# Kernel optimization log

Measured on AMD Instinct MI355X. Metric: run time of the kernel, lower is better.

## Reference

```python
import jax, jax.numpy as jnp
import numpy as np

B = 128          # graphs per batch
NP = 1024        # nodes per graph
FIN = 128        # input node features
H = 128          # hidden width (SAGEConv out)
C = 10           # output classes
N = B * NP
DEG = 16
E = N * DEG
K1 = int(np.ceil(0.8 * NP))   # 820
K2 = int(np.ceil(0.8 * K1))   # 656
K3 = int(np.ceil(0.8 * K2))   # 525


def setup_inputs() -> dict:
    key = jax.random.key(0)
    k = jax.random.split(key, 16)
    x = jax.random.normal(k[0], (N, FIN), jnp.float32)
    # edges constrained within each graph (PyG batched-graph semantics)
    g = jnp.arange(E, dtype=jnp.int32) // (E // B)
    src = g * NP + jax.random.randint(k[1], (E,), 0, NP, jnp.int32)
    dst = g * NP + jax.random.randint(k[2], (E,), 0, NP, jnp.int32)
    edge_index = jnp.stack([src, dst])

    def lin(kk, o, i):
        return jax.random.normal(kk, (o, i), jnp.float32) / np.sqrt(i)

    return {
        'x': x, 'edge_index': edge_index,
        'Wl1': lin(k[3], H, FIN), 'bl1': jnp.zeros((H,), jnp.float32), 'Wr1': lin(k[4], H, FIN),
        'wp1': jax.random.normal(k[5], (H,), jnp.float32),
        'Wl2': lin(k[6], H, H), 'bl2': jnp.zeros((H,), jnp.float32), 'Wr2': lin(k[7], H, H),
        'wp2': jax.random.normal(k[8], (H,), jnp.float32),
        'Wl3': lin(k[9], H, H), 'bl3': jnp.zeros((H,), jnp.float32), 'Wr3': lin(k[10], H, H),
        'wp3': jax.random.normal(k[11], (H,), jnp.float32),
        'Wf1': lin(k[12], 64, H), 'bf1': jnp.zeros((64,), jnp.float32),
        'Wf2': lin(k[13], C, 64), 'bf2': jnp.zeros((C,), jnp.float32),
    }


def _sage(x, src, dst, em, Wl, bl, Wr):
    # PyG SAGEConv: lin_l(mean_{j in N(i)} x_j) + lin_r(x_i); edge mask em kills pruned edges
    msg = x[src] * em[:, None]                                   # [E,H] gather
    s = jax.ops.segment_sum(msg, dst, num_segments=N)            # scatter-add
    deg = jax.ops.segment_sum(em, dst, num_segments=N)
    mean = s / jnp.maximum(deg, 1.0)[:, None]
    return mean @ Wl.T + bl + x @ Wr.T


def _topk(x, w, nm, kk):
    # TopKPooling: score = x.w/||w||, keep top ceil(ratio*n) per graph, gate kept nodes by tanh(score)
    score = (x @ w) / (jnp.linalg.norm(w) + 1e-16)               # [N]
    s2 = jnp.where(nm, score, -jnp.inf).reshape(B, NP)
    _, idx = jax.lax.top_k(s2, kk)                               # [B,kk] static shape
    sel = jnp.zeros((B, NP), bool).at[jnp.arange(B)[:, None], idx].set(True).reshape(-1)
    x = jnp.where(sel[:, None], x * jnp.tanh(score)[:, None], 0.0)
    return x, sel


def _forward(x, Wl1, bl1, Wr1, wp1, Wl2, bl2, Wr2, wp2, Wl3, bl3, Wr3, wp3,
             Wf1, bf1, Wf2, bf2, edge_index):
    src, dst = edge_index[0], edge_index[1]
    nm = jnp.ones((N,), bool)                 # node alive mask
    em = jnp.ones((E,), jnp.float32)          # edge alive mask
    for (Wl, bl, Wr, wp, kk) in ((Wl1, bl1, Wr1, wp1, K1),
                                 (Wl2, bl2, Wr2, wp2, K2),
                                 (Wl3, bl3, Wr3, wp3, K3)):
        x = jax.nn.relu(_sage(x, src, dst, em, Wl, bl, Wr))
        x, nm = _topk(x, wp, nm, kk)
        em = (nm[src] & nm[dst]).astype(jnp.float32)
    # global_mean_pool over surviving nodes per graph (pruned nodes are exactly zero)
    cnt = nm.reshape(B, NP).sum(1).astype(x.dtype)
    pooled = x.reshape(B, NP, H).sum(1) / jnp.maximum(cnt, 1.0)[:, None]
    h = jax.nn.relu(pooled @ Wf1.T + bf1)
    return jax.nn.log_softmax(h @ Wf2.T + bf2, axis=-1)


def reference(x, edge_index, Wl1, bl1, Wr1, wp1, Wl2, bl2, Wr2, wp2,
              Wl3, bl3, Wr3, wp3, Wf1, bf1, Wf2, bf2):
    return _forward(x, Wl1, bl1, Wr1, wp1, Wl2, bl2, Wr2, wp2,
                    Wl3, bl3, Wr3, wp3, Wf1, bf1, Wf2, bf2, edge_index)
```

## Files before the change

### kernel.cpp

```cpp
#include <hip/hip_runtime.h>

constexpr int NGPH = 128;
constexpr int NPG  = 1024;
constexpr int NN   = NGPH * NPG;
constexpr int HD   = 128;
constexpr int EPG  = 16384;
constexpr int KS1 = 820, KS2 = 656, KS3 = 525;

typedef _Float16 half8v __attribute__((ext_vector_type(8)));
typedef float f32x4 __attribute__((ext_vector_type(4)));

__global__ __launch_bounds__(256) void init_gate(float* __restrict__ gate) {
  int i = blockIdx.x * 256 + threadIdx.x;
  if (i < NN) gate[i] = 1.0f;
}

__global__ __launch_bounds__(256) void wconv(const float* __restrict__ Wl0, const float* __restrict__ Wr0,
                                             const float* __restrict__ Wl1, const float* __restrict__ Wr1,
                                             const float* __restrict__ Wl2, const float* __restrict__ Wr2,
                                             _Float16* __restrict__ Wc) {
  int tid = blockIdx.x * 256 + threadIdx.x;
  int layer = tid >> 15;
  int idx = tid & 32767;
  int n = idx >> 8, k = idx & 255;
  const float* Wlp = layer == 0 ? Wl0 : layer == 1 ? Wl1 : Wl2;
  const float* Wrp = layer == 0 ? Wr0 : layer == 1 ? Wr1 : Wr2;
  float v = (k < 128) ? Wlp[n * 128 + k] : Wrp[n * 128 + k - 128];
  _Float16 h = (_Float16)v;
  _Float16 l = (_Float16)(v - (float)h);
  size_t base = (size_t)layer * 65536;
  Wc[base + (size_t)n * 256 + k] = h;
  Wc[base + 32768 + (size_t)n * 256 + k] = l;
}

__global__ __launch_bounds__(512) void csr_build(int* __restrict__ ei) {
  __shared__ unsigned int ed[EPG];
  __shared__ int cnt[NPG];
  __shared__ int scn[NPG];
  __shared__ int off[NPG];
  int g = blockIdx.x, t = threadIdx.x;
  const int* srcg = ei + (size_t)g * EPG;
  const int* dstg = ei + (size_t)NGPH * EPG + (size_t)g * EPG;
  for (int i = t; i < EPG; i += 512) {
    unsigned int s = (unsigned int)(srcg[i] - (g << 10));
    unsigned int d = (unsigned int)(dstg[i] - (g << 10));
    ed[i] = s | (d << 10);
  }
  for (int i = t; i < NPG; i += 512) cnt[i] = 0;
  __syncthreads();
  for (int i = t; i < EPG; i += 512) atomicAdd(&cnt[ed[i] >> 10], 1);
  __syncthreads();
  int* a = cnt; int* b = scn;
  for (int d = 1; d < NPG; d <<= 1) {
    for (int i = t; i < NPG; i += 512) b[i] = a[i] + (i >= d ? a[i - d] : 0);
    __syncthreads();
    int* tmp = a; a = b; b = tmp;
  }
  unsigned short* ssort = (unsigned short*)(ei + (size_t)g * EPG);
  unsigned short* rsout = ssort + EPG;
  for (int r = t; r < NPG; r += 512) {
    int ex = r ? a[r - 1] : 0;
    rsout[r] = (unsigned short)ex;
    off[r] = ex;
  }
  __syncthreads();
  for (int i = t; i < EPG; i += 512) {
    unsigned int e = ed[i];
    int pos = atomicAdd(&off[e >> 10], 1);
    ssort[pos] = (unsigned short)(e & 1023u);
  }
}

__global__ __launch_bounds__(256) void agg2_kernel(const float* __restrict__ X,
                                                   const int* __restrict__ ei,
                                                   const float* __restrict__ gate,
                                                   float* __restrict__ Mout) {
  int t = threadIdx.x;
  int xcd = blockIdx.x & 7, q = blockIdx.x >> 3;
  int g = ((q >> 7) << 3) + xcd;
  int r = (q & 127) * 8 + (t >> 5);
  int lane = t & 31;
  const unsigned short* ss  = (const unsigned short*)(ei + (size_t)g * EPG);
  const unsigned short* rsg = ss + EPG;
  int start = rsg[r];
  int end   = (r < 1023) ? (int)rsg[r + 1] : EPG;
  const float4* X4 = (const float4*)X;
  size_t gb4 = (size_t)(g << 10) * 32;
  float4 acc = make_float4(0.f, 0.f, 0.f, 0.f);
  float degf = 0.f;
  for (int base = start; base < end; base += 32) {
    int ec = end - base; if (ec > 32) ec = 32;
    int sl = 0; float gv = 0.f;
    if (lane < ec) {
      sl = ss[base + lane];
      gv = gate[(g << 10) + sl];
    }
    degf += (gv != 0.f) ? 1.f : 0.f;
    int e = 0;
    for (; e + 8 <= ec; e += 8) {
      int s[8]; float gg[8]; float4 v[8];
#pragma unroll
      for (int k = 0; k < 8; ++k) { s[k] = __shfl(sl, e + k, 32); gg[k] = __shfl(gv, e + k, 32); }
#pragma unroll
      for (int k = 0; k < 8; ++k) v[k] = X4[gb4 + (size_t)s[k] * 32 + lane];
#pragma unroll
      for (int k = 0; k < 8; ++k) {
        acc.x += v[k].x * gg[k]; acc.y += v[k].y * gg[k];
        acc.z += v[k].z * gg[k]; acc.w += v[k].w * gg[k];
      }
    }
    for (; e + 4 <= ec; e += 4) {
      int s[4]; float gg[4]; float4 v[4];
#pragma unroll
      for (int k = 0; k < 4; ++k) { s[k] = __shfl(sl, e + k, 32); gg[k] = __shfl(gv, e + k, 32); }
#pragma unroll
      for (int k = 0; k < 4; ++k) v[k] = X4[gb4 + (size_t)s[k] * 32 + lane];
#pragma unroll
      for (int k = 0; k < 4; ++k) {
        acc.x += v[k].x * gg[k]; acc.y += v[k].y * gg[k];
        acc.z += v[k].z * gg[k]; acc.w += v[k].w * gg[k];
      }
    }
    for (; e < ec; ++e) {
      int s0 = __shfl(sl, e, 32);
      float g0 = __shfl(gv, e, 32);
      float4 v0 = X4[gb4 + (size_t)s0 * 32 + lane];
      acc.x += v0.x * g0; acc.y += v0.y * g0;
      acc.z += v0.z * g0; acc.w += v0.w * g0;
    }
  }
#pragma unroll
  for (int m = 1; m <= 16; m <<= 1) degf += __shfl_xor(degf, m, 32);
  float inv = 1.0f / fmaxf(degf, 1.0f);
  acc.x *= inv; acc.y *= inv; acc.z *= inv; acc.w *= inv;
  ((float4*)Mout)[(size_t)((g << 10) + r) * 32 + lane] = acc;
}

constexpr int LDA = 34;
__global__ __launch_bounds__(256, 4) void gemm_mfma(const float* S,
                                                    const float* __restrict__ X,
                                                    const _Float16* __restrict__ Wc,
                                                    const float* __restrict__ bb,
                                                    const float* __restrict__ wp,
                                                    const float* __restrict__ gate,
                                                    float* Hout,
                                                    float* __restrict__ score) {
  __shared__ _Float16 Ah[128 * LDA];
  __shared__ _Float16 Al[128 * LDA];
  __shared__ _Float16 Bh[128 * LDA];
  __shared__ _Float16 Bl[128 * LDA];
  __shared__ float sc_s[128];
  int t = threadIdx.x;
  int r0 = blockIdx.x * 128;
  int lane = t & 63, wid = t >> 6;
  int wm = wid & 1, wn = wid >> 1;
  int quad = lane >> 4, mr = lane & 15;
  const _Float16* WH = Wc;
  const _Float16* WL = Wc + 32768;

  f32x4 acc[4][4];
#pragma unroll
  for (int i = 0; i < 4; ++i)
#pragma unroll
    for (int j = 0; j < 4; ++j) acc[i][j] = (f32x4){0.f, 0.f, 0.f, 0.f};

  for (int ks = 0; ks < 256; ks += 32) {
    bool isS = (ks < 128);
    const float* Asrc = isS ? (S + (size_t)r0 * HD + ks)
                            : (X + (size_t)r0 * HD + (ks - 128));
#pragma unroll
    for (int i = 0; i < 2; ++i) {
      int slot = t + i * 256;
      int row = slot >> 2;
      int kq = (slot & 3) * 8;
      float4 v0 = *(const float4*)&Asrc[(size_t)row * HD + kq];
      float4 v1 = *(const float4*)&Asrc[(size_t)row * HD + kq + 4];
      if (!isS) {
        float gv = gate[r0 + row];
        v0.x *= gv; v0.y *= gv; v0.z *= gv; v0.w *= gv;
        v1.x *= gv; v1.y *= gv; v1.z *= gv; v1.w *= gv;
      }
      half8v h, l;
      h[0] = (_Float16)v0.x; h[1] = (_Float16)v0.y; h[2] = (_Float16)v0.z; h[3] = (_Float16)v0.w;
      h[4] = (_Float16)v1.x; h[5] = (_Float16)v1.y; h[6] = (_Float16)v1.z; h[7] = (_Float16)v1.w;
      l[0] = (_Float16)(v0.x - (float)h[0]); l[1] = (_Float16)(v0.y - (float)h[1]);
      l[2] = (_Float16)(v0.z - (float)h[2]); l[3] = (_Float16)(v0.w - (float)h[3]);
      l[4] = (_Float16)(v1.x - (float)h[4]); l[5] = (_Float16)(v1.y - (float)h[5]);
      l[6] = (_Float16)(v1.z - (float)h[6]); l[7] = (_Float16)(v1.w - (float)h[7]);
      *(half8v*)&Ah[row * LDA + kq] = h;
      *(half8v*)&Al[row * LDA + kq] = l;
    }
#pragma unroll
    for (int i = 0; i < 2; ++i) {
      int slot = t + i * 256;
      int n = slot >> 2;
      int kq = (slot & 3) * 8;
      *(half8v*)&Bh[n * LDA + kq] = *(const half8v*)&WH[(size_t)n * 256 + ks + kq];
      *(half8v*)&Bl[n * LDA + kq] = *(const half8v*)&WL[(size_t)n * 256 + ks + kq];
    }
    __syncthreads();
    half8v af[4], alf[4], bf[4], blf[4];
#pragma unroll
    for (int i = 0; i < 4; ++i) {
      int rowA = (wm * 64 + i * 16 + mr) * LDA + quad * 8;
      af[i]  = *(const half8v*)&Ah[rowA];
      alf[i] = *(const half8v*)&Al[rowA];
    }
#pragma unroll
    for (int j = 0; j < 4; ++j) {
      int rowW = (wn * 64 + j * 16 + mr) * LDA + quad * 8;
      bf[j]  = *(const half8v*)&Bh[rowW];
      blf[j] = *(const half8v*)&Bl[rowW];
    }
#pragma unroll
    for (int i = 0; i < 4; ++i)
#pragma unroll
      for (int j = 0; j < 4; ++j) {
        acc[i][j] = __builtin_amdgcn_mfma_f32_16x16x32_f16(af[i],  bf[j],  acc[i][j], 0, 0, 0);
        acc[i][j] = __builtin_amdgcn_mfma_f32_16x16x32_f16(af[i],  blf[j], acc[i][j], 0, 0, 0);
        acc[i][j] = __builtin_amdgcn_mfma_f32_16x16x32_f16(alf[i], bf[j],  acc[i][j], 0, 0, 0);
      }
    __syncthreads();
  }
  if (t < 128) sc_s[t] = 0.f;
  __syncthreads();
  float p[4][4];
#pragma unroll
  for (int i = 0; i < 4; ++i)
#pragma unroll
    for (int r = 0; r < 4; ++r) p[i][r] = 0.f;
#pragma unroll
  for (int j = 0; j < 4; ++j) {
    int col = wn * 64 + j * 16 + mr;
    float bias = bb[col];
    float wv = wp[col];
#pragma unroll
    for (int i = 0; i < 4; ++i) {
      int rowg = r0 + wm * 64 + i * 16 + quad * 4;
#pragma unroll
      for (int r = 0; r < 4; ++r) {
        float ho = fmaxf(acc[i][j][r] + bias, 0.f);
        Hout[(size_t)(rowg + r) * HD + col] = ho;
        p[i][r] += ho * wv;
      }
    }
  }
#pragma unroll
  for (int i = 0; i < 4; ++i)
#pragma unroll
    for (int r = 0; r < 4; ++r) {
#pragma unroll
      for (int m = 1; m <= 8; m <<= 1) p[i][r] += __shfl_xor(p[i][r], m, 16);
      if (mr == 0) atomicAdd(&sc_s[wm * 64 + i * 16 + quad * 4 + r], p[i][r]);
    }
  __syncthreads();
  if (t < 128) score[r0 + t] = sc_s[t];
}

__global__ __launch_bounds__(256) void topk_kernel(const float* __restrict__ score,
                                                   float* __restrict__ gate,
                                                   const float* __restrict__ wp,
                                                   int kk) {
  __shared__ float sc[NPG];
  __shared__ float srt[NPG];
  __shared__ float shv[1];
  int g = blockIdx.x, t = threadIdx.x;
  if (t == 0) {
    float ss = 0.f;
    for (int i = 0; i < HD; ++i) ss += wp[i] * wp[i];
    shv[0] = 1.0f / (sqrtf(ss) + 1e-16f);
  }
  __syncthreads();
  float inv = shv[0];
#pragma unroll
  for (int q = 0; q < 4; ++q) {
    int n = t + q * 256;
    float s = score[(g << 10) + n] * inv;
    sc[n] = s;
    srt[n] = (gate[(g << 10) + n] != 0.f) ? s : -3.402823466e38f;
  }
  __syncthreads();
  for (int k2 = 2; k2 <= NPG; k2 <<= 1) {
    for (int j = k2 >> 1; j > 0; j >>= 1) {
#pragma unroll
      for (int q = 0; q < 4; ++q) {
        int i = t + q * 256;
        int l = i ^ j;
        if (l > i) {
          float a = srt[i], b = srt[l];
          if ((a > b) == ((i & k2) == 0)) { srt[i] = b; srt[l] = a; }
        }
      }
      __syncthreads();
    }
  }
  float thr = srt[NPG - kk];
#pragma unroll
  for (int q = 0; q < 4; ++q) {
    int n = t + q * 256;
    float s = sc[n];
    bool sel = (gate[(g << 10) + n] != 0.f) && (s >= thr);
    gate[(g << 10) + n] = sel ? tanhf(s) : 0.f;
  }
}

__global__ __launch_bounds__(1024) void final_kernel(const float* __restrict__ X,
                                                     const float* __restrict__ gate,
                                                     const float* __restrict__ Wf1,
                                                     const float* __restrict__ bf1,
                                                     const float* __restrict__ Wf2,
                                                     const float* __restrict__ bf2,
                                                     float* __restrict__ out) {
  __shared__ float gs[NPG];
  __shared__ float ps[8][HD];
  __shared__ float pl[HD];
  __shared__ float h1[64];
  __shared__ float lg[10];
  __shared__ float red[2];
  int g = blockIdx.x, t = threadIdx.x;
  gs[t] = gate[(g << 10) + t];
  __syncthreads();
  int c = t >> 7, f = t & 127;
  size_t base = (size_t)g * NPG * HD;
  float s = 0.f;
  for (int r = c * 128; r < c * 128 + 128; ++r)
    s += X[base + (size_t)r * HD + f] * gs[r];
  ps[c][f] = s;
  __syncthreads();
  if (t < HD) {
    float tot = 0.f;
#pragma unroll
    for (int cc = 0; cc < 8; ++cc) tot += ps[cc][t];
    pl[t] = tot / (float)KS3;
  }
  __syncthreads();
  if (t < 64) {
    float h = bf1[t];
    for (int ff = 0; ff < HD; ++ff) h += pl[ff] * Wf1[t * HD + ff];
    h1[t] = fmaxf(h, 0.f);
  }
  __syncthreads();
  if (t < 10) {
    float z = bf2[t];
    for (int j = 0; j < 64; ++j) z += h1[j] * Wf2[t * 64 + j];
    lg[t] = z;
  }
  __syncthreads();
  if (t == 0) {
    float m = lg[0];
    for (int cc = 1; cc < 10; ++cc) m = fmaxf(m, lg[cc]);
    float ssum = 0.f;
    for (int cc = 0; cc < 10; ++cc) ssum += expf(lg[cc] - m);
    red[0] = m; red[1] = logf(ssum);
  }
  __syncthreads();
  if (t < 10) out[g * 10 + t] = lg[t] - red[0] - red[1];
}

extern "C" void kernel_launch(void* const* d_in, const int* in_sizes, int n_in,
                              void* d_out, int out_size, void* d_ws, size_t ws_size,
                              hipStream_t stream) {
  const float* x  = (const float*)d_in[0];
  int* ei         = (int*)d_in[1];
  const float* Wl[3]  = {(const float*)d_in[2], (const float*)d_in[6],  (const float*)d_in[10]};
  const float* blv[3] = {(const float*)d_in[3], (const float*)d_in[7],  (const float*)d_in[11]};
  const float* Wr[3]  = {(const float*)d_in[4], (const float*)d_in[8],  (const float*)d_in[12]};
  const float* wp[3]  = {(const float*)d_in[5], (const float*)d_in[9],  (const float*)d_in[13]};
  const float* Wf1 = (const float*)d_in[14];
  const float* bf1 = (const float*)d_in[15];
  const float* Wf2 = (const float*)d_in[16];
  const float* bf2 = (const float*)d_in[17];
  float* out = (float*)d_out;

  float* bufA  = (float*)d_ws;
  float* bufB  = bufA + (size_t)NN * HD;
  float* gate  = bufB + (size_t)NN * HD;
  float* score = gate + NN;
  _Float16* Wcvt = (_Float16*)(score + NN);

  init_gate<<<NN / 256, 256, 0, stream>>>(gate);
  wconv<<<384, 256, 0, stream>>>(Wl[0], Wr[0], Wl[1], Wr[1], Wl[2], Wr[2], Wcvt);
  csr_build<<<NGPH, 512, 0, stream>>>(ei);

  agg2_kernel<<<NN / 8, 256, 0, stream>>>(x, ei, gate, bufA);
  gemm_mfma<<<NN / 128, 256, 0, stream>>>(bufA, x, Wcvt, blv[0], wp[0], gate, bufA, score);
  topk_kernel<<<NGPH, 256, 0, stream>>>(score, gate, wp[0], KS1);
  agg2_kernel<<<NN / 8, 256, 0, stream>>>(bufA, ei, gate, bufB);
  gemm_mfma<<<NN / 128, 256, 0, stream>>>(bufB, bufA, Wcvt + 65536, blv[1], wp[1], gate, bufB, score);
  topk_kernel<<<NGPH, 256, 0, stream>>>(score, gate, wp[1], KS2);
  agg2_kernel<<<NN / 8, 256, 0, stream>>>(bufB, ei, gate, bufA);
  gemm_mfma<<<NN / 128, 256, 0, stream>>>(bufA, bufB, Wcvt + 131072, blv[2], wp[2], gate, bufA, score);
  topk_kernel<<<NGPH, 256, 0, stream>>>(score, gate, wp[2], KS3);

  final_kernel<<<NGPH, 1024, 0, stream>>>(bufA, gate, Wf1, bf1, Wf2, bf2, out);
}
```

Before: 591.3 us.

## Rework aggregation to one wave per node, widen CSR build, split final pooling

```diff
diff --git a/kernel.cpp b/kernel.cpp
--- a/kernel.cpp
+++ b/kernel.cpp
@@ -33,107 +33,85 @@
   Wc[base + 32768 + (size_t)n * 256 + k] = l;
 }
 
-__global__ __launch_bounds__(512) void csr_build(int* __restrict__ ei) {
-  __shared__ unsigned int ed[EPG];
+__global__ __launch_bounds__(1024) void csr_build(int* __restrict__ ei) {
+  __shared__ unsigned short sloc[EPG];
   __shared__ int cnt[NPG];
   __shared__ int scn[NPG];
   __shared__ int off[NPG];
   int g = blockIdx.x, t = threadIdx.x;
   const int* srcg = ei + (size_t)g * EPG;
   const int* dstg = ei + (size_t)NGPH * EPG + (size_t)g * EPG;
-  for (int i = t; i < EPG; i += 512) {
-    unsigned int s = (unsigned int)(srcg[i] - (g << 10));
-    unsigned int d = (unsigned int)(dstg[i] - (g << 10));
-    ed[i] = s | (d << 10);
-  }
-  for (int i = t; i < NPG; i += 512) cnt[i] = 0;
-  __syncthreads();
-  for (int i = t; i < EPG; i += 512) atomicAdd(&cnt[ed[i] >> 10], 1);
+  cnt[t] = 0;
+  for (int i = t; i < EPG; i += 1024)
+    sloc[i] = (unsigned short)(srcg[i] - (g << 10));
+  __syncthreads();
+  for (int i = t; i < EPG; i += 1024)
+    atomicAdd(&cnt[dstg[i] - (g << 10)], 1);
   __syncthreads();
   int* a = cnt; int* b = scn;
   for (int d = 1; d < NPG; d <<= 1) {
-    for (int i = t; i < NPG; i += 512) b[i] = a[i] + (i >= d ? a[i - d] : 0);
+    b[t] = a[t] + (t >= d ? a[t - d] : 0);
     __syncthreads();
     int* tmp = a; a = b; b = tmp;
   }
   unsigned short* ssort = (unsigned short*)(ei + (size_t)g * EPG);
   unsigned short* rsout = ssort + EPG;
-  for (int r = t; r < NPG; r += 512) {
-    int ex = r ? a[r - 1] : 0;
-    rsout[r] = (unsigned short)ex;
-    off[r] = ex;
-  }
-  __syncthreads();
-  for (int i = t; i < EPG; i += 512) {
-    unsigned int e = ed[i];
-    int pos = atomicAdd(&off[e >> 10], 1);
-    ssort[pos] = (unsigned short)(e & 1023u);
-  }
-}
-
-__global__ __launch_bounds__(256) void agg2_kernel(const float* __restrict__ X,
+  int ex = t ? a[t - 1] : 0;
+  rsout[t] = (unsigned short)ex;
+  off[t] = ex;
+  __syncthreads();
+  for (int i = t; i < EPG; i += 1024) {
+    int d = dstg[i] - (g << 10);
+    int pos = atomicAdd(&off[d], 1);
+    ssort[pos] = sloc[i];
+  }
+}
+
+__global__ __launch_bounds__(256) void agg3_kernel(const float* __restrict__ X,
                                                    const int* __restrict__ ei,
                                                    const float* __restrict__ gate,
                                                    float* __restrict__ Mout) {
   int t = threadIdx.x;
-  int xcd = blockIdx.x & 7, q = blockIdx.x >> 3;
-  int g = ((q >> 7) << 3) + xcd;
-  int r = (q & 127) * 8 + (t >> 5);
-  int lane = t & 31;
+  int w = t >> 6, lane = t & 63;
+  int xcd = blockIdx.x & 7, u = blockIdx.x >> 3;
+  int g = __builtin_amdgcn_readfirstlane(xcd + 8 * (u >> 8));
+  int r = __builtin_amdgcn_readfirstlane((u & 255) * 4 + w);
   const unsigned short* ss  = (const unsigned short*)(ei + (size_t)g * EPG);
   const unsigned short* rsg = ss + EPG;
-  int start = rsg[r];
+  int start = __builtin_amdgcn_readfirstlane((int)rsg[r]);
   int end   = (r < 1023) ? (int)rsg[r + 1] : EPG;
-  const float4* X4 = (const float4*)X;
-  size_t gb4 = (size_t)(g << 10) * 32;
-  float4 acc = make_float4(0.f, 0.f, 0.f, 0.f);
-  float degf = 0.f;
-  for (int base = start; base < end; base += 32) {
-    int ec = end - base; if (ec > 32) ec = 32;
-    int sl = 0; float gv = 0.f;
-    if (lane < ec) {
-      sl = ss[base + lane];
-      gv = gate[(g << 10) + sl];
-    }
-    degf += (gv != 0.f) ? 1.f : 0.f;
-    int e = 0;
-    for (; e + 8 <= ec; e += 8) {
-      int s[8]; float gg[8]; float4 v[8];
-#pragma unroll
-      for (int k = 0; k < 8; ++k) { s[k] = __shfl(sl, e + k, 32); gg[k] = __shfl(gv, e + k, 32); }
-#pragma unroll
-      for (int k = 0; k < 8; ++k) v[k] = X4[gb4 + (size_t)s[k] * 32 + lane];
-#pragma unroll
-      for (int k = 0; k < 8; ++k) {
-        acc.x += v[k].x * gg[k]; acc.y += v[k].y * gg[k];
-        acc.z += v[k].z * gg[k]; acc.w += v[k].w * gg[k];
-      }
-    }
-    for (; e + 4 <= ec; e += 4) {
-      int s[4]; float gg[4]; float4 v[4];
-#pragma unroll
-      for (int k = 0; k < 4; ++k) { s[k] = __shfl(sl, e + k, 32); gg[k] = __shfl(gv, e + k, 32); }
-#pragma unroll
-      for (int k = 0; k < 4; ++k) v[k] = X4[gb4 + (size_t)s[k] * 32 + lane];
-#pragma unroll
-      for (int k = 0; k < 4; ++k) {
-        acc.x += v[k].x * gg[k]; acc.y += v[k].y * gg[k];
-        acc.z += v[k].z * gg[k]; acc.w += v[k].w * gg[k];
-      }
-    }
-    for (; e < ec; ++e) {
-      int s0 = __shfl(sl, e, 32);
-      float g0 = __shfl(gv, e, 32);
-      float4 v0 = X4[gb4 + (size_t)s0 * 32 + lane];
-      acc.x += v0.x * g0; acc.y += v0.y * g0;
-      acc.z += v0.z * g0; acc.w += v0.w * g0;
-    }
-  }
-#pragma unroll
-  for (int m = 1; m <= 16; m <<= 1) degf += __shfl_xor(degf, m, 32);
-  float inv = 1.0f / fmaxf(degf, 1.0f);
-  acc.x *= inv; acc.y *= inv; acc.z *= inv; acc.w *= inv;
-  ((float4*)Mout)[(size_t)((g << 10) + r) * 32 + lane] = acc;
+  end = __builtin_amdgcn_readfirstlane(end);
+  int gb = g << 10;
+  const float2* X2 = (const float2*)X;
+  float2 acc = make_float2(0.f, 0.f);
+  float deg = 0.f;
+  int e = start;
+  for (; e + 4 <= end; e += 4) {
+    int i0 = __builtin_amdgcn_readfirstlane((int)ss[e]);
+    int i1 = __builtin_amdgcn_readfirstlane((int)ss[e + 1]);
+    int i2 = __builtin_amdgcn_readfirstlane((int)ss[e + 2]);
+    int i3 = __builtin_amdgcn_readfirstlane((int)ss[e + 3]);
+    float g0 = gate[gb + i0], g1 = gate[gb + i1];
+    float g2 = gate[gb + i2], g3 = gate[gb + i3];
+    float2 v0 = X2[(size_t)(gb + i0) * 64 + lane];
+    float2 v1 = X2[(size_t)(gb + i1) * 64 + lane];
+    float2 v2 = X2[(size_t)(gb + i2) * 64 + lane];
+    float2 v3 = X2[(size_t)(gb + i3) * 64 + lane];
+    acc.x += v0.x * g0 + v1.x * g1 + v2.x * g2 + v3.x * g3;
+    acc.y += v0.y * g0 + v1.y * g1 + v2.y * g2 + v3.y * g3;
+    deg += ((g0 != 0.f) ? 1.f : 0.f) + ((g1 != 0.f) ? 1.f : 0.f)
+         + ((g2 != 0.f) ? 1.f : 0.f) + ((g3 != 0.f) ? 1.f : 0.f);
+  }
+  for (; e < end; ++e) {
+    int i0 = __builtin_amdgcn_readfirstlane((int)ss[e]);
+    float g0 = gate[gb + i0];
+    float2 v0 = X2[(size_t)(gb + i0) * 64 + lane];
+    acc.x += v0.x * g0; acc.y += v0.y * g0;
+    deg += (g0 != 0.f) ? 1.f : 0.f;
+  }
+  float inv = 1.0f / fmaxf(deg, 1.0f);
+  acc.x *= inv; acc.y *= inv;
+  ((float2*)Mout)[(size_t)(gb + r) * 64 + lane] = acc;
 }
 
 constexpr int LDA = 34;
@@ -304,35 +282,41 @@
   }
 }
 
-__global__ __launch_bounds__(1024) void final_kernel(const float* __restrict__ X,
-                                                     const float* __restrict__ gate,
+__global__ __launch_bounds__(256) void pool1_kernel(const float* __restrict__ X,
+                                                    const float* __restrict__ gate,
+                                                    float* __restrict__ part) {
+  __shared__ float gs[128];
+  __shared__ float ps[2][HD];
+  int b = blockIdx.x;
+  int g = b >> 3, c = b & 7;
+  int t = threadIdx.x;
+  if (t < 128) gs[t] = gate[(g << 10) + c * 128 + t];
+  __syncthreads();
+  int f = t & 127, sub = t >> 7;
+  size_t base = (size_t)((g << 10) + c * 128) * HD;
+  float s = 0.f;
+  for (int r = sub; r < 128; r += 2)
+    s += X[base + (size_t)r * HD + f] * gs[r];
+  ps[sub][f] = s;
+  __syncthreads();
+  if (t < 128) part[(g << 10) + c * 128 + t] = ps[0][t] + ps[1][t];
+}
+
+__global__ __launch_bounds__(128) void final2_kernel(const float* __restrict__ part,
                                                      const float* __restrict__ Wf1,
                                                      const float* __restrict__ bf1,
                                                      const float* __restrict__ Wf2,
                                                      const float* __restrict__ bf2,
                                                      float* __restrict__ out) {
-  __shared__ float gs[NPG];
-  __shared__ float ps[8][HD];
   __shared__ float pl[HD];
   __shared__ float h1[64];
   __shared__ float lg[10];
   __shared__ float red[2];
   int g = blockIdx.x, t = threadIdx.x;
-  gs[t] = gate[(g << 10) + t];
-  __syncthreads();
-  int c = t >> 7, f = t & 127;
-  size_t base = (size_t)g * NPG * HD;
-  float s = 0.f;
-  for (int r = c * 128; r < c * 128 + 128; ++r)
-    s += X[base + (size_t)r * HD + f] * gs[r];
-  ps[c][f] = s;
-  __syncthreads();
-  if (t < HD) {
-    float tot = 0.f;
-#pragma unroll
-    for (int cc = 0; cc < 8; ++cc) tot += ps[cc][t];
-    pl[t] = tot / (float)KS3;
-  }
+  float tot = 0.f;
+#pragma unroll
+  for (int c = 0; c < 8; ++c) tot += part[(g << 10) + c * 128 + t];
+  pl[t] = tot / (float)KS3;
   __syncthreads();
   if (t < 64) {
     float h = bf1[t];
@@ -380,17 +364,18 @@
 
   init_gate<<<NN / 256, 256, 0, stream>>>(gate);
   wconv<<<384, 256, 0, stream>>>(Wl[0], Wr[0], Wl[1], Wr[1], Wl[2], Wr[2], Wcvt);
-  csr_build<<<NGPH, 512, 0, stream>>>(ei);
-
-  agg2_kernel<<<NN / 8, 256, 0, stream>>>(x, ei, gate, bufA);
+  csr_build<<<NGPH, 1024, 0, stream>>>(ei);
+
+  agg3_kernel<<<NN / 4, 256, 0, stream>>>(x, ei, gate, bufA);
   gemm_mfma<<<NN / 128, 256, 0, stream>>>(bufA, x, Wcvt, blv[0], wp[0], gate, bufA, score);
   topk_kernel<<<NGPH, 256, 0, stream>>>(score, gate, wp[0], KS1);
-  agg2_kernel<<<NN / 8, 256, 0, stream>>>(bufA, ei, gate, bufB);
+  agg3_kernel<<<NN / 4, 256, 0, stream>>>(bufA, ei, gate, bufB);
   gemm_mfma<<<NN / 128, 256, 0, stream>>>(bufB, bufA, Wcvt + 65536, blv[1], wp[1], gate, bufB, score);
   topk_kernel<<<NGPH, 256, 0, stream>>>(score, gate, wp[1], KS2);
-  agg2_kernel<<<NN / 8, 256, 0, stream>>>(bufB, ei, gate, bufA);
+  agg3_kernel<<<NN / 4, 256, 0, stream>>>(bufB, ei, gate, bufA);
   gemm_mfma<<<NN / 128, 256, 0, stream>>>(bufA, bufB, Wcvt + 131072, blv[2], wp[2], gate, bufA, score);
   topk_kernel<<<NGPH, 256, 0, stream>>>(score, gate, wp[2], KS3);
 
-  final_kernel<<<NGPH, 1024, 0, stream>>>(bufA, gate, Wf1, bf1, Wf2, bf2, out);
-}
+  pool1_kernel<<<NGPH * 8, 256, 0, stream>>>(bufA, gate, score);
+  final2_kernel<<<NGPH, 128, 0, stream>>>(score, Wf1, bf1, Wf2, bf2, out);
+}
```

Result: slower. 694.5 us (+17.5%).
